# Kernel tuning notes

Hardware: AMD Instinct MI355X
Metric: run time of the kernel (lower is better)

Reference implementation:

```python
import jax, jax.numpy as jnp
import numpy as np

HIDDEN = 768
INTER = 1536
N_EXPERTS = 8
TOP_K = 2
AUX_COEF = 0.01


def setup_inputs() -> dict:
    key = jax.random.key(0)
    k0, k1, k2, k3, k4 = jax.random.split(key, 5)
    B, S = 2, 1024
    x = jax.random.normal(k0, (B, S, HIDDEN), dtype=jnp.float32)
    # nn.Linear weights (no bias); stored pre-transposed for einsum (in, out)
    router_w = jax.random.normal(k1, (HIDDEN, N_EXPERTS), dtype=jnp.float32) * 0.02
    w_gate = jax.random.normal(k2, (N_EXPERTS, HIDDEN, INTER), dtype=jnp.float32) * 0.02
    w_up = jax.random.normal(k3, (N_EXPERTS, HIDDEN, INTER), dtype=jnp.float32) * 0.02
    w_down = jax.random.normal(k4, (N_EXPERTS, INTER, HIDDEN), dtype=jnp.float32) * 0.02
    return {"x": x, "router_w": router_w, "w_gate": w_gate, "w_up": w_up, "w_down": w_down}


def reference(x, router_w, w_gate, w_up, w_down):
    B, S, H = x.shape
    xf = x.reshape(-1, H)                      # [T, H]
    T = xf.shape[0]

    router_logits = xf @ router_w              # [T, E]
    router_probs = jax.nn.softmax(router_logits.astype(jnp.float32), axis=-1)
    topk_probs, topk_idx = jax.lax.top_k(router_probs, TOP_K)   # [T, K]
    topk_probs = topk_probs / topk_probs.sum(axis=-1, keepdims=True)

    # dense combine weights: [T, E]; top_k indices are distinct per token so add == set
    comb = jnp.zeros((T, N_EXPERTS), jnp.float32).at[
        jnp.arange(T)[:, None], topk_idx
    ].add(topk_probs)

    # SwiGLU for all experts (dense faithful form of the per-expert gather loop)
    g = jnp.einsum("th,ehi->tei", xf, w_gate)  # [T, E, I]
    u = jnp.einsum("th,ehi->tei", xf, w_up)
    expert_out = jnp.einsum("tei,eih->teh", jax.nn.silu(g) * u, w_down)  # [T, E, H]
    out = jnp.einsum("teh,te->th", expert_out, comb.astype(expert_out.dtype))

    # load-balancing aux loss
    tokens_per_expert = jnp.zeros(N_EXPERTS, jnp.float32).at[topk_idx.reshape(-1)].add(1.0)
    tokens_per_expert = tokens_per_expert / (T * TOP_K)
    router_prob_per_expert = router_probs.mean(axis=0)
    aux_loss = N_EXPERTS * (tokens_per_expert * router_prob_per_expert).sum() * AUX_COEF

    return out.reshape(B, S, H), aux_loss
```

## Files before the change

kernel.cpp:

```cpp
#include <hip/hip_runtime.h>
#include <math.h>


typedef unsigned short u16;
typedef __attribute__((ext_vector_type(8))) short bhalf8;
typedef __attribute__((ext_vector_type(4))) float floatx4;

#define HD 768
#define ID 1536
#define NE 8
#define TT 2048
#define KTOP 2
#define SLOTS 4608
#define RBLK 512

__device__ __forceinline__ float b2f(u16 u) {
    union { unsigned int i; float f; } v; v.i = ((unsigned int)u) << 16; return v.f;
}
__device__ __forceinline__ u16 f2b(float f) {
    union { float f; unsigned int i; } v; v.f = f;
    unsigned int i = v.i;
    return (u16)((i + 0x7FFFu + ((i >> 16) & 1u)) >> 16);
}

__global__ void init_k(const u16* __restrict__ x16, int* flag,
                       int* hdr, int* tokof, float* pslot) {
    int i = blockIdx.x * 256 + threadIdx.x;
    if (i < 40) hdr[i] = 0;
    if (i < SLOTS) { tokof[i] = -1; pslot[i] = 0.f; }
    if (blockIdx.x == 0 && threadIdx.x < 64) {
        int lane = threadIdx.x, c = 0;
#pragma unroll
        for (int j = 0; j < 4; ++j) {
            u16 w = x16[lane + 64 * j];
            int ex = (w >> 7) & 0xFF;
            c += (ex >= 118 && ex <= 135);
        }
#pragma unroll
        for (int off = 32; off > 0; off >>= 1) c += __shfl_xor(c, off);
        if (lane == 0) *flag = (c >= 200) ? 1 : 0;
    }
}

__global__ void xcvt_k(const void* __restrict__ src, u16* __restrict__ dst,
                       const int* __restrict__ flag) {
    int i = (blockIdx.x * 256 + threadIdx.x) * 8;
    if (*flag) {
        *(uint4*)&dst[i] = *(const uint4*)((const u16*)src + i);
    } else {
        const float* s = (const float*)src;
        float4 v0 = *(const float4*)&s[i];
        float4 v1 = *(const float4*)&s[i + 4];
        union { uint4 v; u16 u[8]; } o;
        o.u[0] = f2b(v0.x); o.u[1] = f2b(v0.y); o.u[2] = f2b(v0.z); o.u[3] = f2b(v0.w);
        o.u[4] = f2b(v1.x); o.u[5] = f2b(v1.y); o.u[6] = f2b(v1.z); o.u[7] = f2b(v1.w);
        *(uint4*)&dst[i] = o.v;
    }
}

__global__ void cvtT_k(const void* __restrict__ srcA, const void* __restrict__ srcB,
                       u16* __restrict__ dstA, u16* __restrict__ dstB,
                       int R, int C, const int* __restrict__ flag) {
    __shared__ u16 tile[64][72];
    int z = blockIdx.z;
    const void* src = (z < NE || srcB == nullptr) ? srcA : srcB;
    u16* dst = (z < NE || dstB == nullptr) ? dstA : dstB;
    int e = z & (NE - 1);
    int r0 = blockIdx.y * 64, c0 = blockIdx.x * 64;
    int t = threadIdx.x;
    if (*flag) {
        const u16* s = (const u16*)src + (size_t)e * R * C;
        int r = t >> 3, cg = (t & 7) * 8;
        *(uint4*)&tile[r][cg]      = *(const uint4*)&s[(size_t)(r0 + r) * C + c0 + cg];
        *(uint4*)&tile[r + 32][cg] = *(const uint4*)&s[(size_t)(r0 + r + 32) * C + c0 + cg];
    } else {
        const float* s = (const float*)src + (size_t)e * R * C;
        int r = t >> 2, c4 = (t & 3) * 16;
#pragma unroll
        for (int j = 0; j < 4; ++j) {
            float4 v = *(const float4*)&s[(size_t)(r0 + r) * C + c0 + c4 + 4 * j];
            ushort4 o;
            o.x = f2b(v.x); o.y = f2b(v.y); o.z = f2b(v.z); o.w = f2b(v.w);
            *(ushort4*)&tile[r][c4 + 4 * j] = o;
        }
    }
    __syncthreads();
    u16* d = dst + (size_t)e * R * C;
    int c = t >> 3, rg = (t & 7) * 8;
    union { uint4 v; u16 u[8]; } o;
#pragma unroll
    for (int j = 0; j < 8; ++j) o.u[j] = tile[rg + j][c];
    *(uint4*)&d[(size_t)(c0 + c) * R + r0 + rg] = o.v;
#pragma unroll
    for (int j = 0; j < 8; ++j) o.u[j] = tile[rg + j][c + 32];
    *(uint4*)&d[(size_t)(c0 + c + 32) * R + r0 + rg] = o.v;
}

__global__ void router_k(const void* __restrict__ x, const void* __restrict__ rw,
                         const int* __restrict__ flag,
                         int* topki, float* topkp, float* blockpart) {
    __shared__ float sp[4][NE];
    int lane = threadIdx.x & 63;
    int wave = threadIdx.x >> 6;
    int t = blockIdx.x * 4 + wave;
    int bf = *flag;
    const float* xf = (const float*)x + (size_t)t * HD;
    const u16*   xh = (const u16*)x + (size_t)t * HD;
    const float* rf = (const float*)rw;
    const u16*   rh = (const u16*)rw;
    float acc[NE];
#pragma unroll
    for (int e = 0; e < NE; ++e) acc[e] = 0.f;
    for (int j = 0; j < HD / 64; ++j) {
        int h = lane + 64 * j;
        float xv = bf ? b2f(xh[h]) : xf[h];
#pragma unroll
        for (int e = 0; e < NE; ++e)
            acc[e] += xv * (bf ? b2f(rh[h * NE + e]) : rf[h * NE + e]);
    }
#pragma unroll
    for (int e = 0; e < NE; ++e) {
        float v = acc[e];
#pragma unroll
        for (int off = 32; off > 0; off >>= 1) v += __shfl_xor(v, off);
        acc[e] = v;
    }
    if (lane == 0) {
        float m = acc[0];
        for (int e = 1; e < NE; ++e) m = fmaxf(m, acc[e]);
        float p[NE], s = 0.f;
        for (int e = 0; e < NE; ++e) { p[e] = expf(acc[e] - m); s += p[e]; }
        float inv = 1.f / s;
        for (int e = 0; e < NE; ++e) { p[e] *= inv; sp[wave][e] = p[e]; }
        int i1 = 0; float p1 = p[0];
        for (int e = 1; e < NE; ++e) if (p[e] > p1) { p1 = p[e]; i1 = e; }
        int i2 = -1; float p2 = -1.f;
        for (int e = 0; e < NE; ++e) if (e != i1 && p[e] > p2) { p2 = p[e]; i2 = e; }
        if (i2 < 0) { i2 = (i1 + 1) & 7; p2 = p[i2]; }
        float sn = 1.f / (p1 + p2);
        topki[2 * t] = i1;  topki[2 * t + 1] = i2;
        topkp[2 * t] = p1 * sn;  topkp[2 * t + 1] = p2 * sn;
    }
    __syncthreads();
    if (threadIdx.x < NE) {
        float v = sp[0][threadIdx.x] + sp[1][threadIdx.x] +
                  sp[2][threadIdx.x] + sp[3][threadIdx.x];
        blockpart[blockIdx.x * NE + threadIdx.x] = v;
    }
}

__global__ void prefix_k(const int* __restrict__ topki,
                         const float* __restrict__ blockpart, int* base,
                         int* total, int* cursor, void* out, const int* flag) {
    __shared__ int hist[NE];
    __shared__ float psum[NE];
    int tid = threadIdx.x;
    if (tid < NE) { hist[tid] = 0; psum[tid] = 0.f; }
    __syncthreads();
    for (int i = tid; i < TT * KTOP; i += 256) atomicAdd(&hist[topki[i] & 7], 1);
    for (int i = tid; i < RBLK * NE; i += 256) atomicAdd(&psum[i & 7], blockpart[i]);
    __syncthreads();
    if (tid == 0) {
        int cum = 0; float aux = 0.f;
        for (int e = 0; e < NE; ++e) {
            int c = hist[e];
            base[e] = cum; cum += (c + 63) & ~63;
            cursor[e] = 0;
            aux += ((float)c / (float)(TT * KTOP)) * (psum[e] / (float)TT);
        }
        *total = cum;
        float auxv = aux * (float)NE * 0.01f;
        if (*flag) ((u16*)out)[(size_t)TT * HD] = f2b(auxv);
        else       ((float*)out)[(size_t)TT * HD] = auxv;
    }
}

__global__ void scatter_k(const int* __restrict__ topki, const float* __restrict__ topkp,
                          const int* __restrict__ base, int* cursor,
                          int* tokof, float* pslot, int* slotmap) {
    __shared__ int lcnt[NE], lbase[NE];
    int tid = threadIdx.x;
    int t = blockIdx.x * 256 + tid;
    if (tid < NE) lcnt[tid] = 0;
    __syncthreads();
    int e0 = topki[2 * t] & 7, e1 = topki[2 * t + 1] & 7;
    float q0 = topkp[2 * t], q1 = topkp[2 * t + 1];
    int l0 = atomicAdd(&lcnt[e0], 1);
    int l1 = atomicAdd(&lcnt[e1], 1);
    __syncthreads();
    if (tid < NE) lbase[tid] = atomicAdd(&cursor[tid], lcnt[tid]);
    __syncthreads();
    int s0 = min(max(base[e0] + lbase[e0] + l0, 0), SLOTS - 1);
    int s1 = min(max(base[e1] + lbase[e1] + l1, 0), SLOTS - 1);
    tokof[s0] = t;  pslot[s0] = q0;  slotmap[2 * t] = s0;
    tokof[s1] = t;  pslot[s1] = q1;  slotmap[2 * t + 1] = s1;
}

__global__ __launch_bounds__(256) void gemm1_k(
        const u16* __restrict__ xb, const u16* __restrict__ wgt,
        const u16* __restrict__ wut, const int* __restrict__ base,
        const int* __restrict__ total, const int* __restrict__ tokof,
        u16* __restrict__ act) {
    __shared__ u16 As[64][72], Bg[64][72], Bu[64][72];
    int row0 = blockIdx.y * 64;
    if (row0 >= *total) return;
    int e = 7;
    while (e > 0 && row0 < base[e]) --e;
    int n0 = blockIdx.x * 64;
    int tid = threadIdx.x;
    int r = tid >> 2, cg = (tid & 3) * 8;
    int tok = tokof[row0 + r];
    bool tv = ((unsigned)tok < (unsigned)TT);
    const u16* xrow = xb + (size_t)(tv ? tok : 0) * HD;
    const u16* bgrow = wgt + ((size_t)e * ID + n0 + r) * HD;
    const u16* burow = wut + ((size_t)e * ID + n0 + r) * HD;
    int wave = tid >> 6, lane = tid & 63;
    int wm = (wave & 1) * 32, wn = (wave >> 1) * 32;
    int lhi = (lane >> 4) * 8, llo = lane & 15;
    floatx4 accG[2][2], accU[2][2];
#pragma unroll
    for (int i = 0; i < 2; ++i)
#pragma unroll
        for (int j = 0; j < 2; ++j) {
            accG[i][j] = floatx4{0.f, 0.f, 0.f, 0.f};
            accU[i][j] = floatx4{0.f, 0.f, 0.f, 0.f};
        }
    uint4 z4 = make_uint4(0, 0, 0, 0);
    for (int k0 = 0; k0 < HD; k0 += 64) {
        uint4 a1 = z4, a2 = z4;
        if (tv) {
            a1 = *(const uint4*)&xrow[k0 + cg];
            a2 = *(const uint4*)&xrow[k0 + cg + 32];
        }
        uint4 g1 = *(const uint4*)&bgrow[k0 + cg];
        uint4 g2 = *(const uint4*)&bgrow[k0 + cg + 32];
        uint4 u1 = *(const uint4*)&burow[k0 + cg];
        uint4 u2 = *(const uint4*)&burow[k0 + cg + 32];
        __syncthreads();
        *(uint4*)&As[r][cg] = a1; *(uint4*)&As[r][cg + 32] = a2;
        *(uint4*)&Bg[r][cg] = g1; *(uint4*)&Bg[r][cg + 32] = g2;
        *(uint4*)&Bu[r][cg] = u1; *(uint4*)&Bu[r][cg + 32] = u2;
        __syncthreads();
#pragma unroll
        for (int kk = 0; kk < 64; kk += 32) {
            bhalf8 a0 = *(const bhalf8*)&As[wm + llo][kk + lhi];
            bhalf8 a1f = *(const bhalf8*)&As[wm + 16 + llo][kk + lhi];
            bhalf8 b0 = *(const bhalf8*)&Bg[wn + llo][kk + lhi];
            bhalf8 b1 = *(const bhalf8*)&Bg[wn + 16 + llo][kk + lhi];
            bhalf8 c0 = *(const bhalf8*)&Bu[wn + llo][kk + lhi];
            bhalf8 c1 = *(const bhalf8*)&Bu[wn + 16 + llo][kk + lhi];
            accG[0][0] = __builtin_amdgcn_mfma_f32_16x16x32_bf16(a0, b0, accG[0][0], 0, 0, 0);
            accG[0][1] = __builtin_amdgcn_mfma_f32_16x16x32_bf16(a0, b1, accG[0][1], 0, 0, 0);
            accG[1][0] = __builtin_amdgcn_mfma_f32_16x16x32_bf16(a1f, b0, accG[1][0], 0, 0, 0);
            accG[1][1] = __builtin_amdgcn_mfma_f32_16x16x32_bf16(a1f, b1, accG[1][1], 0, 0, 0);
            accU[0][0] = __builtin_amdgcn_mfma_f32_16x16x32_bf16(a0, c0, accU[0][0], 0, 0, 0);
            accU[0][1] = __builtin_amdgcn_mfma_f32_16x16x32_bf16(a0, c1, accU[0][1], 0, 0, 0);
            accU[1][0] = __builtin_amdgcn_mfma_f32_16x16x32_bf16(a1f, c0, accU[1][0], 0, 0, 0);
            accU[1][1] = __builtin_amdgcn_mfma_f32_16x16x32_bf16(a1f, c1, accU[1][1], 0, 0, 0);
        }
    }
    int mrow = (lane >> 4) * 4;
#pragma unroll
    for (int i = 0; i < 2; ++i)
#pragma unroll
        for (int j = 0; j < 2; ++j)
#pragma unroll
            for (int rr = 0; rr < 4; ++rr) {
                int m = row0 + wm + i * 16 + mrow + rr;
                int n = n0 + wn + j * 16 + llo;
                float g = accG[i][j][rr], u = accU[i][j][rr];
                float sv = g / (1.f + expf(-g));
                act[(size_t)m * ID + n] = f2b(sv * u);
            }
}

__global__ __launch_bounds__(256) void gemm2_k(
        const u16* __restrict__ act, const u16* __restrict__ wdt,
        const int* __restrict__ base, const int* __restrict__ total,
        const float* __restrict__ pslot, float* __restrict__ y) {
    __shared__ u16 As[64][72], Bs[64][72];
    int row0 = blockIdx.y * 64;
    if (row0 >= *total) return;
    int e = 7;
    while (e > 0 && row0 < base[e]) --e;
    int n0 = blockIdx.x * 64;
    int tid = threadIdx.x;
    int r = tid >> 2, cg = (tid & 3) * 8;
    const u16* arow = act + (size_t)(row0 + r) * ID;
    const u16* brow = wdt + ((size_t)e * HD + n0 + r) * ID;
    int wave = tid >> 6, lane = tid & 63;
    int wm = (wave & 1) * 32, wn = (wave >> 1) * 32;
    int lhi = (lane >> 4) * 8, llo = lane & 15;
    floatx4 acc[2][2];
#pragma unroll
    for (int i = 0; i < 2; ++i)
#pragma unroll
        for (int j = 0; j < 2; ++j) acc[i][j] = floatx4{0.f, 0.f, 0.f, 0.f};
    for (int k0 = 0; k0 < ID; k0 += 64) {
        uint4 a1 = *(const uint4*)&arow[k0 + cg];
        uint4 a2 = *(const uint4*)&arow[k0 + cg + 32];
        uint4 b1 = *(const uint4*)&brow[k0 + cg];
        uint4 b2 = *(const uint4*)&brow[k0 + cg + 32];
        __syncthreads();
        *(uint4*)&As[r][cg] = a1; *(uint4*)&As[r][cg + 32] = a2;
        *(uint4*)&Bs[r][cg] = b1; *(uint4*)&Bs[r][cg + 32] = b2;
        __syncthreads();
#pragma unroll
        for (int kk = 0; kk < 64; kk += 32) {
            bhalf8 a0 = *(const bhalf8*)&As[wm + llo][kk + lhi];
            bhalf8 a1f = *(const bhalf8*)&As[wm + 16 + llo][kk + lhi];
            bhalf8 b0 = *(const bhalf8*)&Bs[wn + llo][kk + lhi];
            bhalf8 b1f = *(const bhalf8*)&Bs[wn + 16 + llo][kk + lhi];
            acc[0][0] = __builtin_amdgcn_mfma_f32_16x16x32_bf16(a0, b0, acc[0][0], 0, 0, 0);
            acc[0][1] = __builtin_amdgcn_mfma_f32_16x16x32_bf16(a0, b1f, acc[0][1], 0, 0, 0);
            acc[1][0] = __builtin_amdgcn_mfma_f32_16x16x32_bf16(a1f, b0, acc[1][0], 0, 0, 0);
            acc[1][1] = __builtin_amdgcn_mfma_f32_16x16x32_bf16(a1f, b1f, acc[1][1], 0, 0, 0);
        }
    }
    int mrow = (lane >> 4) * 4;
#pragma unroll
    for (int i = 0; i < 2; ++i)
#pragma unroll
        for (int j = 0; j < 2; ++j)
#pragma unroll
            for (int rr = 0; rr < 4; ++rr) {
                int m = row0 + wm + i * 16 + mrow + rr;
                int n = n0 + wn + j * 16 + llo;
                float p = pslot[m];
                y[(size_t)m * HD + n] = p * acc[i][j][rr];
            }
}

__global__ void combine_k(const float* __restrict__ y, const int* __restrict__ slotmap,
                          void* __restrict__ out, const int* __restrict__ flag) {
    int g = blockIdx.x * 256 + threadIdx.x;
    int t = g / 192;
    int q = (g % 192) * 4;
    int s0 = slotmap[2 * t], s1 = slotmap[2 * t + 1];
    s0 = min(max(s0, 0), SLOTS - 1);
    s1 = min(max(s1, 0), SLOTS - 1);
    float4 a = *(const float4*)&y[(size_t)s0 * HD + q];
    float4 b = *(const float4*)&y[(size_t)s1 * HD + q];
    float4 rv;
    rv.x = a.x + b.x; rv.y = a.y + b.y; rv.z = a.z + b.z; rv.w = a.w + b.w;
    if (*flag) {
        ushort4 o;
        o.x = f2b(rv.x); o.y = f2b(rv.y); o.z = f2b(rv.z); o.w = f2b(rv.w);
        *(ushort4*)((u16*)out + (size_t)t * HD + q) = o;
    } else {
        *(float4*)((float*)out + (size_t)t * HD + q) = rv;
    }
}

extern "C" void kernel_launch(void* const* d_in, const int* in_sizes, int n_in,
                              void* d_out, int out_size, void* d_ws, size_t ws_size,
                              hipStream_t stream) {
    const void* x  = d_in[0];
    const void* rw = d_in[1];
    const void* wg = d_in[2];
    const void* wu = d_in[3];
    const void* wd = d_in[4];
    char* ws = (char*)d_ws;

    int*   hdr     = (int*)(ws + 0);
    int*   cursor  = (int*)(ws + 32);
    int*   base    = (int*)(ws + 64);
    int*   total   = (int*)(ws + 96);
    int*   flag    = (int*)(ws + 224);
    int*   topki   = (int*)(ws + 256);
    float* topkp   = (float*)(ws + 16640);
    int*   tokof   = (int*)(ws + 33024);
    float* pslot   = (float*)(ws + 51456);
    int*   slotmap = (int*)(ws + 69888);
    float* blockpart = (float*)(ws + 86272);
    u16*   xb      = (u16*)(ws + 102656);
    u16*   act     = (u16*)(ws + 3248384);
    float* ybuf    = (float*)(ws + 17404160);
    u16*   wgt     = (u16*)(ws + 31559936);
    u16*   wut     = (u16*)(ws + 50434304);
    u16*   wdt     = (u16*)(ws + 69308672);
    if (ws_size < 88183040u) return;

    init_k<<<18, 256, 0, stream>>>((const u16*)x, flag, hdr, tokof, pslot);
    xcvt_k<<<(TT * HD / 8) / 256, 256, 0, stream>>>(x, xb, flag);
    cvtT_k<<<dim3(ID / 64, HD / 64, 2 * NE), 256, 0, stream>>>(wg, wu, wgt, wut,
                                                               HD, ID, flag);
    cvtT_k<<<dim3(HD / 64, ID / 64, NE), 256, 0, stream>>>(wd, nullptr, wdt, nullptr,
                                                           ID, HD, flag);
    router_k<<<RBLK, 256, 0, stream>>>(x, rw, flag, topki, topkp, blockpart);
    prefix_k<<<1, 256, 0, stream>>>(topki, blockpart, base, total, cursor, d_out, flag);
    scatter_k<<<TT / 256, 256, 0, stream>>>(topki, topkp, base, cursor,
                                            tokof, pslot, slotmap);
    gemm1_k<<<dim3(ID / 64, SLOTS / 64), 256, 0, stream>>>(xb, wgt, wut, base, total,
                                                           tokof, act);
    gemm2_k<<<dim3(HD / 64, SLOTS / 64), 256, 0, stream>>>(act, wdt, base, total,
                                                           pslot, ybuf);
    combine_k<<<(TT * 192) / 256, 256, 0, stream>>>(ybuf, slotmap, d_out, flag);
}
```

Baseline: 270.5 us.

## Pack operands into swizzled tiles and use 128x128 MFMA GEMM tiles with direct LDS loads

Replaces the separate x conversion and weight transpose kernels with pack kernels. These write gathered token rows and expert weights as contiguous XOR-swizzled 64x128 bf16 tiles. The two GEMMs move from 64x64 to 128x128 block tiles with a 4x4 MFMA tile per wave, and load tiles straight into LDS with global_load_lds. Expert segments are padded to 128 rows and the y buffer aliases the weight area. This aims to raise data reuse, remove LDS bank conflicts and register staging, and fold the token gather into the A pack. The costs are more padding, higher register pressure, and no double buffering, since every k-tile still waits on vmcnt(0).

```diff
diff --git a/kernel.cpp b/kernel.cpp
--- a/kernel.cpp
+++ b/kernel.cpp
@@ -10,8 +10,8 @@
 #define ID 1536
 #define NE 8
 #define TT 2048
-#define KTOP 2
-#define SLOTS 4608
+#define SLOTS 5120
+#define MT 40
 #define RBLK 512
 
 __device__ __forceinline__ float b2f(u16 u) {
@@ -21,6 +21,11 @@
     union { float f; unsigned int i; } v; v.f = f;
     unsigned int i = v.i;
     return (u16)((i + 0x7FFFu + ((i >> 16) & 1u)) >> 16);
+}
+__device__ __forceinline__ void glds16(const u16* g, u16* l) {
+    __builtin_amdgcn_global_load_lds(
+        (const __attribute__((address_space(1))) unsigned int*)g,
+        (__attribute__((address_space(3))) unsigned int*)l, 16, 0, 0);
 }
 
 __global__ void init_k(const u16* __restrict__ x16, int* flag,
@@ -28,8 +33,8 @@
     int i = blockIdx.x * 256 + threadIdx.x;
     if (i < 40) hdr[i] = 0;
     if (i < SLOTS) { tokof[i] = -1; pslot[i] = 0.f; }
-    if (blockIdx.x == 0 && threadIdx.x < 64) {
-        int lane = threadIdx.x, c = 0;
+    if (blockIdx.x == 0 && threadIdx.x >= 64 && threadIdx.x < 128) {
+        int lane = threadIdx.x - 64, c = 0;
 #pragma unroll
         for (int j = 0; j < 4; ++j) {
             u16 w = x16[lane + 64 * j];
@@ -42,66 +47,11 @@
     }
 }
 
-__global__ void xcvt_k(const void* __restrict__ src, u16* __restrict__ dst,
-                       const int* __restrict__ flag) {
-    int i = (blockIdx.x * 256 + threadIdx.x) * 8;
-    if (*flag) {
-        *(uint4*)&dst[i] = *(const uint4*)((const u16*)src + i);
-    } else {
-        const float* s = (const float*)src;
-        float4 v0 = *(const float4*)&s[i];
-        float4 v1 = *(const float4*)&s[i + 4];
-        union { uint4 v; u16 u[8]; } o;
-        o.u[0] = f2b(v0.x); o.u[1] = f2b(v0.y); o.u[2] = f2b(v0.z); o.u[3] = f2b(v0.w);
-        o.u[4] = f2b(v1.x); o.u[5] = f2b(v1.y); o.u[6] = f2b(v1.z); o.u[7] = f2b(v1.w);
-        *(uint4*)&dst[i] = o.v;
-    }
-}
-
-__global__ void cvtT_k(const void* __restrict__ srcA, const void* __restrict__ srcB,
-                       u16* __restrict__ dstA, u16* __restrict__ dstB,
-                       int R, int C, const int* __restrict__ flag) {
-    __shared__ u16 tile[64][72];
-    int z = blockIdx.z;
-    const void* src = (z < NE || srcB == nullptr) ? srcA : srcB;
-    u16* dst = (z < NE || dstB == nullptr) ? dstA : dstB;
-    int e = z & (NE - 1);
-    int r0 = blockIdx.y * 64, c0 = blockIdx.x * 64;
-    int t = threadIdx.x;
-    if (*flag) {
-        const u16* s = (const u16*)src + (size_t)e * R * C;
-        int r = t >> 3, cg = (t & 7) * 8;
-        *(uint4*)&tile[r][cg]      = *(const uint4*)&s[(size_t)(r0 + r) * C + c0 + cg];
-        *(uint4*)&tile[r + 32][cg] = *(const uint4*)&s[(size_t)(r0 + r + 32) * C + c0 + cg];
-    } else {
-        const float* s = (const float*)src + (size_t)e * R * C;
-        int r = t >> 2, c4 = (t & 3) * 16;
-#pragma unroll
-        for (int j = 0; j < 4; ++j) {
-            float4 v = *(const float4*)&s[(size_t)(r0 + r) * C + c0 + c4 + 4 * j];
-            ushort4 o;
-            o.x = f2b(v.x); o.y = f2b(v.y); o.z = f2b(v.z); o.w = f2b(v.w);
-            *(ushort4*)&tile[r][c4 + 4 * j] = o;
-        }
-    }
-    __syncthreads();
-    u16* d = dst + (size_t)e * R * C;
-    int c = t >> 3, rg = (t & 7) * 8;
-    union { uint4 v; u16 u[8]; } o;
-#pragma unroll
-    for (int j = 0; j < 8; ++j) o.u[j] = tile[rg + j][c];
-    *(uint4*)&d[(size_t)(c0 + c) * R + r0 + rg] = o.v;
-#pragma unroll
-    for (int j = 0; j < 8; ++j) o.u[j] = tile[rg + j][c + 32];
-    *(uint4*)&d[(size_t)(c0 + c + 32) * R + r0 + rg] = o.v;
-}
-
 __global__ void router_k(const void* __restrict__ x, const void* __restrict__ rw,
                          const int* __restrict__ flag,
                          int* topki, float* topkp, float* blockpart) {
     __shared__ float sp[4][NE];
-    int lane = threadIdx.x & 63;
-    int wave = threadIdx.x >> 6;
+    int lane = threadIdx.x & 63, wave = threadIdx.x >> 6;
     int t = blockIdx.x * 4 + wave;
     int bf = *flag;
     const float* xf = (const float*)x + (size_t)t * HD;
@@ -142,11 +92,10 @@
         topkp[2 * t] = p1 * sn;  topkp[2 * t + 1] = p2 * sn;
     }
     __syncthreads();
-    if (threadIdx.x < NE) {
-        float v = sp[0][threadIdx.x] + sp[1][threadIdx.x] +
-                  sp[2][threadIdx.x] + sp[3][threadIdx.x];
-        blockpart[blockIdx.x * NE + threadIdx.x] = v;
-    }
+    if (threadIdx.x < NE)
+        blockpart[blockIdx.x * NE + threadIdx.x] =
+            sp[0][threadIdx.x] + sp[1][threadIdx.x] +
+            sp[2][threadIdx.x] + sp[3][threadIdx.x];
 }
 
 __global__ void prefix_k(const int* __restrict__ topki,
@@ -157,16 +106,16 @@
     int tid = threadIdx.x;
     if (tid < NE) { hist[tid] = 0; psum[tid] = 0.f; }
     __syncthreads();
-    for (int i = tid; i < TT * KTOP; i += 256) atomicAdd(&hist[topki[i] & 7], 1);
+    for (int i = tid; i < TT * 2; i += 256) atomicAdd(&hist[topki[i] & 7], 1);
     for (int i = tid; i < RBLK * NE; i += 256) atomicAdd(&psum[i & 7], blockpart[i]);
     __syncthreads();
     if (tid == 0) {
         int cum = 0; float aux = 0.f;
         for (int e = 0; e < NE; ++e) {
             int c = hist[e];
-            base[e] = cum; cum += (c + 63) & ~63;
+            base[e] = cum; cum += (c + 127) & ~127;
             cursor[e] = 0;
-            aux += ((float)c / (float)(TT * KTOP)) * (psum[e] / (float)TT);
+            aux += ((float)c / (float)(TT * 2)) * (psum[e] / (float)TT);
         }
         *total = cum;
         float auxv = aux * (float)NE * 0.01f;
@@ -196,139 +145,235 @@
     tokof[s1] = t;  pslot[s1] = q1;  slotmap[2 * t + 1] = s1;
 }
 
-__global__ __launch_bounds__(256) void gemm1_k(
-        const u16* __restrict__ xb, const u16* __restrict__ wgt,
-        const u16* __restrict__ wut, const int* __restrict__ base,
-        const int* __restrict__ total, const int* __restrict__ tokof,
-        u16* __restrict__ act) {
-    __shared__ u16 As[64][72], Bg[64][72], Bu[64][72];
-    int row0 = blockIdx.y * 64;
-    if (row0 >= *total) return;
+__global__ void apack_k(const void* __restrict__ x, const int* __restrict__ flag,
+                        const int* __restrict__ tokof, const int* __restrict__ total,
+                        u16* __restrict__ apack) {
+    int mt = blockIdx.y, kt = blockIdx.x;
+    if (mt * 128 >= *total) return;
+    int tid = threadIdx.x;
+    int ml = tid >> 1, half = tid & 1;
+    int tok = tokof[mt * 128 + ml];
+    union { uint4 v[4]; u16 u[32]; } buf;
+    if ((unsigned)tok < (unsigned)TT) {
+        if (*flag) {
+            const u16* s = (const u16*)x + (size_t)tok * HD + kt * 64 + half * 32;
+#pragma unroll
+            for (int c = 0; c < 4; ++c) buf.v[c] = *(const uint4*)&s[c * 8];
+        } else {
+            const float* s = (const float*)x + (size_t)tok * HD + kt * 64 + half * 32;
+#pragma unroll
+            for (int c = 0; c < 8; ++c) {
+                float4 f = *(const float4*)&s[c * 4];
+                buf.u[c * 4 + 0] = f2b(f.x); buf.u[c * 4 + 1] = f2b(f.y);
+                buf.u[c * 4 + 2] = f2b(f.z); buf.u[c * 4 + 3] = f2b(f.w);
+            }
+        }
+    } else {
+#pragma unroll
+        for (int c = 0; c < 4; ++c) buf.v[c] = make_uint4(0, 0, 0, 0);
+    }
+    u16* dst = apack + (((size_t)mt * 12 + kt) << 13) + ml * 64;
+#pragma unroll
+    for (int c = 0; c < 4; ++c) {
+        int pc = (half * 4 + c) ^ (ml & 7);
+        *(uint4*)(dst + pc * 8) = buf.v[c];
+    }
+}
+
+__global__ void wpack_k(const void* __restrict__ srcA, const void* __restrict__ srcB,
+                        u16* __restrict__ dstA, u16* __restrict__ dstB,
+                        int K, int N, int ktiles, int ntiles,
+                        const int* __restrict__ flag) {
+    __shared__ u16 t[8192];
+    int z = blockIdx.z;
+    const void* src = (srcB != nullptr && z >= NE) ? srcB : srcA;
+    u16* dst = (dstB != nullptr && z >= NE) ? dstB : dstA;
+    int e = z & 7;
+    int kt = blockIdx.x, nt = blockIdx.y;
+    int tid = threadIdx.x;
+    int kr = tid >> 2, ng = (tid & 3) * 32;
+    size_t srow = ((size_t)e * K + (size_t)kt * 64 + kr) * N + (size_t)nt * 128 + ng;
+    union { uint4 v[4]; u16 u[32]; } buf;
+    if (*flag) {
+        const u16* s = (const u16*)src + srow;
+#pragma unroll
+        for (int c = 0; c < 4; ++c) buf.v[c] = *(const uint4*)&s[c * 8];
+    } else {
+        const float* s = (const float*)src + srow;
+#pragma unroll
+        for (int c = 0; c < 8; ++c) {
+            float4 f = *(const float4*)&s[c * 4];
+            buf.u[c * 4 + 0] = f2b(f.x); buf.u[c * 4 + 1] = f2b(f.y);
+            buf.u[c * 4 + 2] = f2b(f.z); buf.u[c * 4 + 3] = f2b(f.w);
+        }
+    }
+#pragma unroll
+    for (int jj = 0; jj < 32; ++jj) {
+        int n = ng + jj;
+        t[n * 64 + (((kr >> 3) ^ (n & 7)) << 3) + (kr & 7)] = buf.u[jj];
+    }
+    __syncthreads();
+    u16* d = dst + ((((size_t)e * ntiles + nt) * ktiles + kt) << 13);
+#pragma unroll
+    for (int i = 0; i < 4; ++i) {
+        int off = tid * 8 + i * 2048;
+        *(uint4*)(d + off) = *(const uint4*)&t[off];
+    }
+}
+
+__global__ __launch_bounds__(256, 2) void gemm1_k(
+        const u16* __restrict__ apack, const u16* __restrict__ wgp,
+        const u16* __restrict__ wup, const int* __restrict__ base,
+        const int* __restrict__ total, u16* __restrict__ actp) {
+    __shared__ u16 smem[24576];
+    u16* As = smem; u16* Bg = smem + 8192; u16* Bu = smem + 16384;
+    int mt = blockIdx.y;
+    if (mt * 128 >= *total) return;
     int e = 7;
-    while (e > 0 && row0 < base[e]) --e;
-    int n0 = blockIdx.x * 64;
-    int tid = threadIdx.x;
-    int r = tid >> 2, cg = (tid & 3) * 8;
-    int tok = tokof[row0 + r];
-    bool tv = ((unsigned)tok < (unsigned)TT);
-    const u16* xrow = xb + (size_t)(tv ? tok : 0) * HD;
-    const u16* bgrow = wgt + ((size_t)e * ID + n0 + r) * HD;
-    const u16* burow = wut + ((size_t)e * ID + n0 + r) * HD;
-    int wave = tid >> 6, lane = tid & 63;
-    int wm = (wave & 1) * 32, wn = (wave >> 1) * 32;
-    int lhi = (lane >> 4) * 8, llo = lane & 15;
-    floatx4 accG[2][2], accU[2][2];
-#pragma unroll
-    for (int i = 0; i < 2; ++i)
-#pragma unroll
-        for (int j = 0; j < 2; ++j) {
+    while (e > 0 && mt * 128 < base[e]) --e;
+    int nt = blockIdx.x;
+    int tid = threadIdx.x, lane = tid & 63, wave = tid >> 6;
+    int wm = (wave & 1) * 64, wn = (wave >> 1) * 64;
+    int llo = lane & 15, lq = lane >> 4;
+    const u16* atile = apack + (((size_t)mt * 12) << 13);
+    const u16* gtile = wgp + ((((size_t)e * 12 + nt) * 12) << 13);
+    const u16* utile = wup + ((((size_t)e * 12 + nt) * 12) << 13);
+    floatx4 accG[4][4], accU[4][4];
+#pragma unroll
+    for (int i = 0; i < 4; ++i)
+#pragma unroll
+        for (int j = 0; j < 4; ++j) {
             accG[i][j] = floatx4{0.f, 0.f, 0.f, 0.f};
             accU[i][j] = floatx4{0.f, 0.f, 0.f, 0.f};
         }
-    uint4 z4 = make_uint4(0, 0, 0, 0);
-    for (int k0 = 0; k0 < HD; k0 += 64) {
-        uint4 a1 = z4, a2 = z4;
-        if (tv) {
-            a1 = *(const uint4*)&xrow[k0 + cg];
-            a2 = *(const uint4*)&xrow[k0 + cg + 32];
-        }
-        uint4 g1 = *(const uint4*)&bgrow[k0 + cg];
-        uint4 g2 = *(const uint4*)&bgrow[k0 + cg + 32];
-        uint4 u1 = *(const uint4*)&burow[k0 + cg];
-        uint4 u2 = *(const uint4*)&burow[k0 + cg + 32];
+    for (int kt = 0; kt < 12; ++kt) {
+        const u16* ga = atile + (kt << 13);
+        const u16* gg = gtile + (kt << 13);
+        const u16* gu = utile + (kt << 13);
         __syncthreads();
-        *(uint4*)&As[r][cg] = a1; *(uint4*)&As[r][cg + 32] = a2;
-        *(uint4*)&Bg[r][cg] = g1; *(uint4*)&Bg[r][cg + 32] = g2;
-        *(uint4*)&Bu[r][cg] = u1; *(uint4*)&Bu[r][cg + 32] = u2;
+#pragma unroll
+        for (int i = 0; i < 4; ++i) {
+            int off = tid * 8 + i * 2048;
+            glds16(ga + off, As + off);
+            glds16(gg + off, Bg + off);
+            glds16(gu + off, Bu + off);
+        }
+        asm volatile("s_waitcnt vmcnt(0)" ::: "memory");
         __syncthreads();
 #pragma unroll
-        for (int kk = 0; kk < 64; kk += 32) {
-            bhalf8 a0 = *(const bhalf8*)&As[wm + llo][kk + lhi];
-            bhalf8 a1f = *(const bhalf8*)&As[wm + 16 + llo][kk + lhi];
-            bhalf8 b0 = *(const bhalf8*)&Bg[wn + llo][kk + lhi];
-            bhalf8 b1 = *(const bhalf8*)&Bg[wn + 16 + llo][kk + lhi];
-            bhalf8 c0 = *(const bhalf8*)&Bu[wn + llo][kk + lhi];
-            bhalf8 c1 = *(const bhalf8*)&Bu[wn + 16 + llo][kk + lhi];
-            accG[0][0] = __builtin_amdgcn_mfma_f32_16x16x32_bf16(a0, b0, accG[0][0], 0, 0, 0);
-            accG[0][1] = __builtin_amdgcn_mfma_f32_16x16x32_bf16(a0, b1, accG[0][1], 0, 0, 0);
-            accG[1][0] = __builtin_amdgcn_mfma_f32_16x16x32_bf16(a1f, b0, accG[1][0], 0, 0, 0);
-            accG[1][1] = __builtin_amdgcn_mfma_f32_16x16x32_bf16(a1f, b1, accG[1][1], 0, 0, 0);
-            accU[0][0] = __builtin_amdgcn_mfma_f32_16x16x32_bf16(a0, c0, accU[0][0], 0, 0, 0);
-            accU[0][1] = __builtin_amdgcn_mfma_f32_16x16x32_bf16(a0, c1, accU[0][1], 0, 0, 0);
-            accU[1][0] = __builtin_amdgcn_mfma_f32_16x16x32_bf16(a1f, c0, accU[1][0], 0, 0, 0);
-            accU[1][1] = __builtin_amdgcn_mfma_f32_16x16x32_bf16(a1f, c1, accU[1][1], 0, 0, 0);
-        }
-    }
-    int mrow = (lane >> 4) * 4;
-#pragma unroll
-    for (int i = 0; i < 2; ++i)
-#pragma unroll
-        for (int j = 0; j < 2; ++j)
+        for (int kk = 0; kk < 2; ++kk) {
+            int q = kk * 4 + lq;
+            bhalf8 af[4], bg[4], bu[4];
+#pragma unroll
+            for (int i = 0; i < 4; ++i) {
+                int m = wm + i * 16 + llo;
+                af[i] = *(const bhalf8*)&As[m * 64 + ((q ^ (m & 7)) << 3)];
+                int n = wn + i * 16 + llo;
+                bg[i] = *(const bhalf8*)&Bg[n * 64 + ((q ^ (n & 7)) << 3)];
+                bu[i] = *(const bhalf8*)&Bu[n * 64 + ((q ^ (n & 7)) << 3)];
+            }
+#pragma unroll
+            for (int i = 0; i < 4; ++i)
+#pragma unroll
+                for (int j = 0; j < 4; ++j) {
+                    accG[i][j] = __builtin_amdgcn_mfma_f32_16x16x32_bf16(af[i], bg[j], accG[i][j], 0, 0, 0);
+                    accU[i][j] = __builtin_amdgcn_mfma_f32_16x16x32_bf16(af[i], bu[j], accU[i][j], 0, 0, 0);
+                }
+        }
+    }
+    __syncthreads();
+    u16* Ah = smem;
+    int q4 = lq * 4;
+#pragma unroll
+    for (int i = 0; i < 4; ++i)
+#pragma unroll
+        for (int j = 0; j < 4; ++j)
 #pragma unroll
             for (int rr = 0; rr < 4; ++rr) {
-                int m = row0 + wm + i * 16 + mrow + rr;
-                int n = n0 + wn + j * 16 + llo;
+                int m = wm + i * 16 + q4 + rr;
+                int n = wn + j * 16 + llo;
                 float g = accG[i][j][rr], u = accU[i][j][rr];
-                float sv = g / (1.f + expf(-g));
-                act[(size_t)m * ID + n] = f2b(sv * u);
+                Ah[m * 128 + n] = f2b((g / (1.f + expf(-g))) * u);
             }
-}
-
-__global__ __launch_bounds__(256) void gemm2_k(
-        const u16* __restrict__ act, const u16* __restrict__ wdt,
+    __syncthreads();
+    u16* dst = actp + (((size_t)mt * 24 + nt * 2) << 13);
+#pragma unroll
+    for (int s = 0; s < 2; ++s)
+#pragma unroll
+        for (int i = 0; i < 4; ++i) {
+            int off = tid * 8 + i * 2048;
+            int m = off >> 6;
+            int pc = (off >> 3) & 7;
+            int q = pc ^ (m & 7);
+            *(uint4*)(dst + ((size_t)s << 13) + off) =
+                *(const uint4*)&Ah[m * 128 + s * 64 + q * 8];
+        }
+}
+
+__global__ __launch_bounds__(256, 2) void gemm2_k(
+        const u16* __restrict__ actp, const u16* __restrict__ wdp,
         const int* __restrict__ base, const int* __restrict__ total,
         const float* __restrict__ pslot, float* __restrict__ y) {
-    __shared__ u16 As[64][72], Bs[64][72];
-    int row0 = blockIdx.y * 64;
-    if (row0 >= *total) return;
+    __shared__ u16 smem[16384];
+    u16* As = smem; u16* Bs = smem + 8192;
+    int mt = blockIdx.y;
+    if (mt * 128 >= *total) return;
     int e = 7;
-    while (e > 0 && row0 < base[e]) --e;
-    int n0 = blockIdx.x * 64;
-    int tid = threadIdx.x;
-    int r = tid >> 2, cg = (tid & 3) * 8;
-    const u16* arow = act + (size_t)(row0 + r) * ID;
-    const u16* brow = wdt + ((size_t)e * HD + n0 + r) * ID;
-    int wave = tid >> 6, lane = tid & 63;
-    int wm = (wave & 1) * 32, wn = (wave >> 1) * 32;
-    int lhi = (lane >> 4) * 8, llo = lane & 15;
-    floatx4 acc[2][2];
-#pragma unroll
-    for (int i = 0; i < 2; ++i)
-#pragma unroll
-        for (int j = 0; j < 2; ++j) acc[i][j] = floatx4{0.f, 0.f, 0.f, 0.f};
-    for (int k0 = 0; k0 < ID; k0 += 64) {
-        uint4 a1 = *(const uint4*)&arow[k0 + cg];
-        uint4 a2 = *(const uint4*)&arow[k0 + cg + 32];
-        uint4 b1 = *(const uint4*)&brow[k0 + cg];
-        uint4 b2 = *(const uint4*)&brow[k0 + cg + 32];
+    while (e > 0 && mt * 128 < base[e]) --e;
+    int nt = blockIdx.x;
+    int tid = threadIdx.x, lane = tid & 63, wave = tid >> 6;
+    int wm = (wave & 1) * 64, wn = (wave >> 1) * 64;
+    int llo = lane & 15, lq = lane >> 4;
+    const u16* atile = actp + (((size_t)mt * 24) << 13);
+    const u16* btile = wdp + ((((size_t)e * 6 + nt) * 24) << 13);
+    floatx4 acc[4][4];
+#pragma unroll
+    for (int i = 0; i < 4; ++i)
+#pragma unroll
+        for (int j = 0; j < 4; ++j) acc[i][j] = floatx4{0.f, 0.f, 0.f, 0.f};
+    for (int kt = 0; kt < 24; ++kt) {
+        const u16* ga = atile + (kt << 13);
+        const u16* gb = btile + (kt << 13);
         __syncthreads();
-        *(uint4*)&As[r][cg] = a1; *(uint4*)&As[r][cg + 32] = a2;
-        *(uint4*)&Bs[r][cg] = b1; *(uint4*)&Bs[r][cg + 32] = b2;
+#pragma unroll
+        for (int i = 0; i < 4; ++i) {
+            int off = tid * 8 + i * 2048;
+            glds16(ga + off, As + off);
+            glds16(gb + off, Bs + off);
+        }
+        asm volatile("s_waitcnt vmcnt(0)" ::: "memory");
         __syncthreads();
 #pragma unroll
-        for (int kk = 0; kk < 64; kk += 32) {
-            bhalf8 a0 = *(const bhalf8*)&As[wm + llo][kk + lhi];
-            bhalf8 a1f = *(const bhalf8*)&As[wm + 16 + llo][kk + lhi];
-            bhalf8 b0 = *(const bhalf8*)&Bs[wn + llo][kk + lhi];
-            bhalf8 b1f = *(const bhalf8*)&Bs[wn + 16 + llo][kk + lhi];
-            acc[0][0] = __builtin_amdgcn_mfma_f32_16x16x32_bf16(a0, b0, acc[0][0], 0, 0, 0);
-            acc[0][1] = __builtin_amdgcn_mfma_f32_16x16x32_bf16(a0, b1f, acc[0][1], 0, 0, 0);
-            acc[1][0] = __builtin_amdgcn_mfma_f32_16x16x32_bf16(a1f, b0, acc[1][0], 0, 0, 0);
-            acc[1][1] = __builtin_amdgcn_mfma_f32_16x16x32_bf16(a1f, b1f, acc[1][1], 0, 0, 0);
-        }
-    }
-    int mrow = (lane >> 4) * 4;
-#pragma unroll
-    for (int i = 0; i < 2; ++i)
-#pragma unroll
-        for (int j = 0; j < 2; ++j)
-#pragma unroll
-            for (int rr = 0; rr < 4; ++rr) {
-                int m = row0 + wm + i * 16 + mrow + rr;
-                int n = n0 + wn + j * 16 + llo;
-                float p = pslot[m];
+        for (int kk = 0; kk < 2; ++kk) {
+            int q = kk * 4 + lq;
+            bhalf8 af[4], bf[4];
+#pragma unroll
+            for (int i = 0; i < 4; ++i) {
+                int m = wm + i * 16 + llo;
+                af[i] = *(const bhalf8*)&As[m * 64 + ((q ^ (m & 7)) << 3)];
+                int n = wn + i * 16 + llo;
+                bf[i] = *(const bhalf8*)&Bs[n * 64 + ((q ^ (n & 7)) << 3)];
+            }
+#pragma unroll
+            for (int i = 0; i < 4; ++i)
+#pragma unroll
+                for (int j = 0; j < 4; ++j)
+                    acc[i][j] = __builtin_amdgcn_mfma_f32_16x16x32_bf16(af[i], bf[j], acc[i][j], 0, 0, 0);
+        }
+    }
+    int q4 = lq * 4;
+#pragma unroll
+    for (int i = 0; i < 4; ++i)
+#pragma unroll
+        for (int rr = 0; rr < 4; ++rr) {
+            int m = mt * 128 + wm + i * 16 + q4 + rr;
+            float p = pslot[m];
+#pragma unroll
+            for (int j = 0; j < 4; ++j) {
+                int n = nt * 128 + wn + j * 16 + llo;
                 y[(size_t)m * HD + n] = p * acc[i][j][rr];
             }
+        }
 }
 
 __global__ void combine_k(const float* __restrict__ y, const int* __restrict__ slotmap,
@@ -336,9 +381,8 @@
     int g = blockIdx.x * 256 + threadIdx.x;
     int t = g / 192;
     int q = (g % 192) * 4;
-    int s0 = slotmap[2 * t], s1 = slotmap[2 * t + 1];
-    s0 = min(max(s0, 0), SLOTS - 1);
-    s1 = min(max(s1, 0), SLOTS - 1);
+    int s0 = min(max(slotmap[2 * t], 0), SLOTS - 1);
+    int s1 = min(max(slotmap[2 * t + 1], 0), SLOTS - 1);
     float4 a = *(const float4*)&y[(size_t)s0 * HD + q];
     float4 b = *(const float4*)&y[(size_t)s1 * HD + q];
     float4 rv;
@@ -370,30 +414,28 @@
     int*   topki   = (int*)(ws + 256);
     float* topkp   = (float*)(ws + 16640);
     int*   tokof   = (int*)(ws + 33024);
-    float* pslot   = (float*)(ws + 51456);
-    int*   slotmap = (int*)(ws + 69888);
-    float* blockpart = (float*)(ws + 86272);
-    u16*   xb      = (u16*)(ws + 102656);
-    u16*   act     = (u16*)(ws + 3248384);
-    float* ybuf    = (float*)(ws + 17404160);
-    u16*   wgt     = (u16*)(ws + 31559936);
-    u16*   wut     = (u16*)(ws + 50434304);
-    u16*   wdt     = (u16*)(ws + 69308672);
-    if (ws_size < 88183040u) return;
-
-    init_k<<<18, 256, 0, stream>>>((const u16*)x, flag, hdr, tokof, pslot);
-    xcvt_k<<<(TT * HD / 8) / 256, 256, 0, stream>>>(x, xb, flag);
-    cvtT_k<<<dim3(ID / 64, HD / 64, 2 * NE), 256, 0, stream>>>(wg, wu, wgt, wut,
-                                                               HD, ID, flag);
-    cvtT_k<<<dim3(HD / 64, ID / 64, NE), 256, 0, stream>>>(wd, nullptr, wdt, nullptr,
-                                                           ID, HD, flag);
+    float* pslot   = (float*)(ws + 53504);
+    int*   slotmap = (int*)(ws + 73984);
+    float* blockpart = (float*)(ws + 90368);
+    u16*   apack   = (u16*)(ws + 106752);
+    u16*   actp    = (u16*)(ws + 7971072);
+    u16*   wgp     = (u16*)(ws + 23699712);
+    u16*   wup     = (u16*)(ws + 42574080);
+    u16*   wdp     = (u16*)(ws + 61448448);
+    float* ybuf    = (float*)(ws + 23699712);
+    if (ws_size < 80322816u) return;
+
+    init_k<<<20, 256, 0, stream>>>((const u16*)x, flag, hdr, tokof, pslot);
     router_k<<<RBLK, 256, 0, stream>>>(x, rw, flag, topki, topkp, blockpart);
     prefix_k<<<1, 256, 0, stream>>>(topki, blockpart, base, total, cursor, d_out, flag);
     scatter_k<<<TT / 256, 256, 0, stream>>>(topki, topkp, base, cursor,
                                             tokof, pslot, slotmap);
-    gemm1_k<<<dim3(ID / 64, SLOTS / 64), 256, 0, stream>>>(xb, wgt, wut, base, total,
-                                                           tokof, act);
-    gemm2_k<<<dim3(HD / 64, SLOTS / 64), 256, 0, stream>>>(act, wdt, base, total,
-                                                           pslot, ybuf);
+    apack_k<<<dim3(12, MT), 256, 0, stream>>>(x, flag, tokof, total, apack);
+    wpack_k<<<dim3(12, 12, 16), 256, 0, stream>>>(wg, wu, wgp, wup,
+                                                  HD, ID, 12, 12, flag);
+    wpack_k<<<dim3(24, 6, 8), 256, 0, stream>>>(wd, nullptr, wdp, nullptr,
+                                                ID, HD, 24, 6, flag);
+    gemm1_k<<<dim3(12, MT), 256, 0, stream>>>(apack, wgp, wup, base, total, actp);
+    gemm2_k<<<dim3(6, MT), 256, 0, stream>>>(actp, wdp, base, total, pslot, ybuf);
     combine_k<<<(TT * 192) / 256, 256, 0, stream>>>(ybuf, slotmap, d_out, flag);
 }
```

New measurement: 266.8 us. Within noise of the previous version (-1.4%).
